# Optimization experiments

Hardware: AMD Instinct MI355X
Metric: run time of the kernel (lower is better)

The kernel has to match this reference:

```python
import jax, jax.numpy as jnp
import numpy as np

EPS = 1e-4


def setup_inputs() -> dict:
    key = jax.random.key(0)
    k1, k2, k3, k4, k5 = jax.random.split(key, 5)
    N, M, F = 2048, 2048, 128
    embeds = jax.random.uniform(k1, (N, F), dtype=jnp.float32)
    base_embeds = jax.random.normal(k2, (M, F), dtype=jnp.float32)
    base_rewards = jax.random.normal(k3, (M,), dtype=jnp.float32)
    # torch Linear(num_feat, num_feat, bias=False) / Linear(num_feat, 1, bias=False)
    # stored here as [in, out] for x @ W convention
    W1 = jax.random.normal(k4, (F, F), dtype=jnp.float32) / np.sqrt(F)
    w2 = jax.random.normal(k5, (F, 1), dtype=jnp.float32) / np.sqrt(F)
    return {"embeds": embeds, "base_embeds": base_embeds,
            "base_rewards": base_rewards, "W1": W1, "w2": w2}


def reference(embeds, base_embeds, base_rewards, W1, w2):
    # pairwise differences: [N, M, F]
    diff = embeds[:, None, :] - base_embeds[None, :, :]
    # tiny MLP distance kernel: Linear -> ELU -> Linear, abs
    h = jax.nn.elu(jnp.einsum('nmf,fg->nmg', diff, W1))
    dist = jnp.abs(jnp.einsum('nmg,go->nmo', h, w2)[:, :, 0])  # [N, M]
    # inverse-distance normalized weights
    dist_w = 1.0 / (dist + EPS)
    dist_w = dist_w / jnp.sum(dist_w, axis=1, keepdims=True)
    rewards = jnp.sum(dist_w * base_rewards[None, :], axis=1)  # [N]
    return rewards
```

## Files before the change

kernel.cpp:

```cpp
#include <hip/hip_runtime.h>
#include <hip/hip_bf16.h>

#define F      128
#define NROWS  2048
#define MROWS  2048
#define MT     32
#define LOG2E  1.44269504088896340736f

typedef float f32x4 __attribute__((ext_vector_type(4)));

__global__ __launch_bounds__(256) void proj_kernel(
    const float* __restrict__ embeds, const float* __restrict__ base,
    const float* __restrict__ W1, const float* __restrict__ w2,
    float* __restrict__ PA, float* __restrict__ BT4,
    float* __restrict__ w2sum)
{
    const int tid = threadIdx.x;
    const int sub = tid >> 7;
    const int g   = tid & 127;
    const int row = blockIdx.x * 2 + sub;

    __shared__ float xs[2][F];
    {
        const float* src = (row < NROWS) ? &embeds[(size_t)row * F]
                                         : &base[(size_t)(row - NROWS) * F];
        xs[sub][g] = src[g];
    }
    __syncthreads();

    float acc = 0.0f;
#pragma unroll 8
    for (int f = 0; f < F; ++f)
        acc = fmaf(xs[sub][f], W1[f * F + g], acc);

    const float wv = w2[g];
    const int   ch = g >> 3, o = g & 7;
    if (row < NROWS) {
        float* dst = PA + (size_t)row * 256 + ch * 16 + o;
        dst[0] = (acc + 1.0f) * wv;
        dst[8] = __builtin_amdgcn_exp2f(acc * LOG2E) * wv;
    } else {
        const int m  = row - NROWS;
        const int f0 = o, f1 = 8 + o;
        BT4[((size_t)(ch * 4 + (f0 >> 2)) * 2048 + m) * 4 + (f0 & 3)] = -acc * wv;
        BT4[((size_t)(ch * 4 + (f1 >> 2)) * 2048 + m) * 4 + (f1 & 3)] =
            __builtin_amdgcn_exp2f(-acc * LOG2E);
    }

    if (blockIdx.x == 0 && tid < 64) {
        float s = w2[tid] + w2[tid + 64];
#pragma unroll
        for (int k = 1; k < 64; k <<= 1) s += __shfl_xor(s, k);
        if (tid == 0) *w2sum = s;
    }
}

__global__ __launch_bounds__(256, 4) void pair_kernel(
    const float* __restrict__ PA, const float* __restrict__ BT4,
    const float* __restrict__ w2, const float* __restrict__ w2sum_p,
    const float* __restrict__ brew, float* __restrict__ partials)
{
    const int lane = threadIdx.x & 63;
    const int wv   = __builtin_amdgcn_readfirstlane(threadIdx.x >> 6);
    const int nt   = blockIdx.x, mt = blockIdx.y;
    const int n0   = nt * 32 + wv * 8;
    const int m0   = mt * 64;

    const float* bbase = BT4 + (size_t)(m0 + lane) * 4;

    float acc[8];
#pragma unroll
    for (int r = 0; r < 8; ++r) acc[r] = 0.0f;

    f32x4 rB[4], rBn[4];
#pragma unroll
    for (int q = 0; q < 4; ++q)
        rB[q] = *(const f32x4*)&bbase[(size_t)q * 8192];

#pragma unroll 1
    for (int ch = 0; ch < 16; ++ch) {
        if (ch < 15) {
#pragma unroll
            for (int q = 0; q < 4; ++q)
                rBn[q] = *(const f32x4*)&bbase[(size_t)((ch + 1) * 4 + q) * 8192];
        }
        const float* w2c = w2 + ch * 8;
        const float w0 = w2c[0], w1 = w2c[1], w2_ = w2c[2], w3 = w2c[3];
        const float w4 = w2c[4], w5 = w2c[5], w6 = w2c[6], w7 = w2c[7];

#pragma unroll
        for (int r = 0; r < 8; ++r) {
            const float* ar = PA + (size_t)(n0 + r) * 256 + ch * 16;
            const f32x4 a10 = *(const f32x4*)&ar[0];
            const f32x4 a11 = *(const f32x4*)&ar[4];
            const f32x4 ae0 = *(const f32x4*)&ar[8];
            const f32x4 ae1 = *(const f32x4*)&ar[12];

            const float s0 = __builtin_amdgcn_fmed3f(a10[0] + rB[0][0], ae0[0] * rB[2][0], w0);
            const float s1 = __builtin_amdgcn_fmed3f(a10[1] + rB[0][1], ae0[1] * rB[2][1], w1);
            const float s2 = __builtin_amdgcn_fmed3f(a10[2] + rB[0][2], ae0[2] * rB[2][2], w2_);
            const float s3 = __builtin_amdgcn_fmed3f(a10[3] + rB[0][3], ae0[3] * rB[2][3], w3);
            const float s4 = __builtin_amdgcn_fmed3f(a11[0] + rB[1][0], ae1[0] * rB[3][0], w4);
            const float s5 = __builtin_amdgcn_fmed3f(a11[1] + rB[1][1], ae1[1] * rB[3][1], w5);
            const float s6 = __builtin_amdgcn_fmed3f(a11[2] + rB[1][2], ae1[2] * rB[3][2], w6);
            const float s7 = __builtin_amdgcn_fmed3f(a11[3] + rB[1][3], ae1[3] * rB[3][3], w7);
            acc[r] += ((s0 + s1) + (s2 + s3)) + ((s4 + s5) + (s6 + s7));
        }
#pragma unroll
        for (int q = 0; q < 4; ++q) rB[q] = rBn[q];
    }

    const float w2sum = *w2sum_p;
    const float rv    = brew[m0 + lane];

#pragma unroll
    for (int r = 0; r < 8; ++r) {
        const float dist = fabsf(acc[r] - w2sum);
        const float wgt  = 1.0f / (dist + 1e-4f);
        float sw  = wgt;
        float swr = wgt * rv;
#pragma unroll
        for (int k = 1; k < 64; k <<= 1) {
            sw  += __shfl_xor(sw, k);
            swr += __shfl_xor(swr, k);
        }
        if (lane == 0) {
            const int n = n0 + r;
            partials[((size_t)n * MT + mt) * 2 + 0] = sw;
            partials[((size_t)n * MT + mt) * 2 + 1] = swr;
        }
    }
}

__global__ __launch_bounds__(256) void finalize_kernel(
    const float* __restrict__ partials, float* __restrict__ out)
{
    const int n = blockIdx.x * 256 + threadIdx.x;
    if (n < NROWS) {
        float sw = 0.0f, swr = 0.0f;
#pragma unroll
        for (int t = 0; t < MT; ++t) {
            sw  += partials[((size_t)n * MT + t) * 2 + 0];
            swr += partials[((size_t)n * MT + t) * 2 + 1];
        }
        out[n] = swr / sw;
    }
}

extern "C" void kernel_launch(void* const* d_in, const int* in_sizes, int n_in,
                              void* d_out, int out_size, void* d_ws, size_t ws_size,
                              hipStream_t stream)
{
    const float* embeds       = (const float*)d_in[0];
    const float* base_embeds  = (const float*)d_in[1];
    const float* base_rewards = (const float*)d_in[2];
    const float* W1           = (const float*)d_in[3];
    const float* w2           = (const float*)d_in[4];
    float* out = (float*)d_out;

    float* partials = (float*)d_ws;
    float* PA  = partials + (size_t)NROWS * MT * 2;
    float* BT4 = PA + (size_t)NROWS * 256;
    float* w2s = BT4 + (size_t)64 * 2048 * 4;

    proj_kernel<<<(NROWS + MROWS) / 2, 256, 0, stream>>>(
        embeds, base_embeds, W1, w2, PA, BT4, w2s);

    dim3 grid2(NROWS / 32, MROWS / 64);
    pair_kernel<<<grid2, 256, 0, stream>>>(PA, BT4, w2, w2s, base_rewards, partials);

    finalize_kernel<<<(NROWS + 255) / 256, 256, 0, stream>>>(partials, out);
}
```

Measured before the change: 83.59 us.

## Retile pair kernel to 4x4 register micro-tiles with LDS-staged A via global_load_lds

Restructures the pairwise kernel so each lane computes a 4x4 block of (n,m) pairs instead of 8 rows by one column. A-side rows are staged into per-wave double-buffered LDS with direct global-to-LDS loads, and B is loaded in split halves and software-pipelined across chunks. Each block now covers 64x64 pairs, and the reduction uses 16-lane shuffles. The aim is to cut redundant global loads of PA and raise arithmetic intensity, at the cost of more registers, explicit vmcnt waits and a more complex LDS indexing scheme.

```diff
diff --git a/kernel.cpp b/kernel.cpp
--- a/kernel.cpp
+++ b/kernel.cpp
@@ -8,6 +8,12 @@
 #define LOG2E  1.44269504088896340736f
 
 typedef float f32x4 __attribute__((ext_vector_type(4)));
+
+__device__ __forceinline__ void gload16(const float* g, float* l) {
+    __builtin_amdgcn_global_load_lds(
+        (const __attribute__((address_space(1))) void*)g,
+        (__attribute__((address_space(3))) void*)l, 16, 0, 0);
+}
 
 __global__ __launch_bounds__(256) void proj_kernel(
     const float* __restrict__ embeds, const float* __restrict__ base,
@@ -60,72 +66,112 @@
     const float* __restrict__ w2, const float* __restrict__ w2sum_p,
     const float* __restrict__ brew, float* __restrict__ partials)
 {
-    const int lane = threadIdx.x & 63;
-    const int wv   = __builtin_amdgcn_readfirstlane(threadIdx.x >> 6);
-    const int nt   = blockIdx.x, mt = blockIdx.y;
-    const int n0   = nt * 32 + wv * 8;
-    const int m0   = mt * 64;
-
-    const float* bbase = BT4 + (size_t)(m0 + lane) * 4;
-
-    float acc[8];
-#pragma unroll
-    for (int r = 0; r < 8; ++r) acc[r] = 0.0f;
-
-    f32x4 rB[4], rBn[4];
-#pragma unroll
-    for (int q = 0; q < 4; ++q)
-        rB[q] = *(const f32x4*)&bbase[(size_t)q * 8192];
+    __shared__ float slds[4 * 640];
+
+    const int tid = threadIdx.x;
+    const int w   = tid >> 6, l = tid & 63;
+    const int nt  = blockIdx.x, mt = blockIdx.y;
+    const int n0  = nt * 64,    m0 = mt * 64;
+    const int trl = (l >> 4) & 3;
+    const int tc  = l & 15;
+    const int wbase = w * 640;
+
+    const float* sA0;
+    const float* sA1;
+    {
+        const int s = l, r = s / 5;
+        int rs = s - r * 5; if (rs == 4) rs = 0;
+        sA0 = PA + (size_t)(n0 + 4 * w + (r & 3) + 16 * (r >> 2)) * 256 + rs * 4;
+    }
+    {
+        const int s = 64 + l, r = s / 5;
+        int rs = s - r * 5; if (rs == 4) rs = 0;
+        sA1 = PA + (size_t)(n0 + 4 * w + (r & 3) + 16 * (r >> 2)) * 256 + rs * 4;
+    }
+
+#define STAGE_A(CH, BUF) {                                                     \
+    float* db = &slds[wbase + (BUF) * 320];                                    \
+    gload16(sA0 + (CH) * 16, db);                                              \
+    if (l < 16) gload16(sA1 + (CH) * 16, db + 256); }
+
+    const float* bcol = BT4 + (size_t)(m0 + tc) * 4;
+#define LOADB(D1, DE, CH, H) {                                                 \
+    _Pragma("unroll")                                                          \
+    for (int j = 0; j < 4; ++j) {                                              \
+        D1[j] = *(const f32x4*)&bcol[(size_t)((CH) * 4 + (H)) * 8192 + 64 * j];     \
+        DE[j] = *(const f32x4*)&bcol[(size_t)((CH) * 4 + 2 + (H)) * 8192 + 64 * j]; \
+    } }
+
+    float acc[4][4];
+#pragma unroll
+    for (int i = 0; i < 4; ++i)
+#pragma unroll
+        for (int j = 0; j < 4; ++j) acc[i][j] = 0.0f;
+
+#define COMPUTE_H(CH, H, B1, BE, BUF) {                                        \
+    const float wq0 = w2[(CH) * 8 + (H) * 4 + 0];                              \
+    const float wq1 = w2[(CH) * 8 + (H) * 4 + 1];                              \
+    const float wq2 = w2[(CH) * 8 + (H) * 4 + 2];                              \
+    const float wq3 = w2[(CH) * 8 + (H) * 4 + 3];                              \
+    _Pragma("unroll")                                                          \
+    for (int i = 0; i < 4; ++i) {                                              \
+        const float* ap = &slds[wbase + (BUF) * 320 + (i * 4 + trl) * 20 + (H) * 4]; \
+        const f32x4 a1 = *(const f32x4*)ap;                                    \
+        const f32x4 ae = *(const f32x4*)(ap + 8);                              \
+        _Pragma("unroll")                                                      \
+        for (int j = 0; j < 4; ++j) {                                          \
+            const float s0 = __builtin_amdgcn_fmed3f(a1[0] + B1[j][0], ae[0] * BE[j][0], wq0); \
+            const float s1 = __builtin_amdgcn_fmed3f(a1[1] + B1[j][1], ae[1] * BE[j][1], wq1); \
+            const float s2 = __builtin_amdgcn_fmed3f(a1[2] + B1[j][2], ae[2] * BE[j][2], wq2); \
+            const float s3 = __builtin_amdgcn_fmed3f(a1[3] + B1[j][3], ae[3] * BE[j][3], wq3); \
+            acc[i][j] += (s0 + s1) + (s2 + s3);                                \
+        }                                                                      \
+    } }
+
+    f32x4 bX1[4], bXe[4], bY1[4], bYe[4];
+
+    LOADB(bX1, bXe, 0, 0)
+    STAGE_A(0, 0)
+    asm volatile("s_waitcnt vmcnt(0)" ::: "memory");
 
 #pragma unroll 1
     for (int ch = 0; ch < 16; ++ch) {
-        if (ch < 15) {
-#pragma unroll
-            for (int q = 0; q < 4; ++q)
-                rBn[q] = *(const f32x4*)&bbase[(size_t)((ch + 1) * 4 + q) * 8192];
-        }
-        const float* w2c = w2 + ch * 8;
-        const float w0 = w2c[0], w1 = w2c[1], w2_ = w2c[2], w3 = w2c[3];
-        const float w4 = w2c[4], w5 = w2c[5], w6 = w2c[6], w7 = w2c[7];
-
-#pragma unroll
-        for (int r = 0; r < 8; ++r) {
-            const float* ar = PA + (size_t)(n0 + r) * 256 + ch * 16;
-            const f32x4 a10 = *(const f32x4*)&ar[0];
-            const f32x4 a11 = *(const f32x4*)&ar[4];
-            const f32x4 ae0 = *(const f32x4*)&ar[8];
-            const f32x4 ae1 = *(const f32x4*)&ar[12];
-
-            const float s0 = __builtin_amdgcn_fmed3f(a10[0] + rB[0][0], ae0[0] * rB[2][0], w0);
-            const float s1 = __builtin_amdgcn_fmed3f(a10[1] + rB[0][1], ae0[1] * rB[2][1], w1);
-            const float s2 = __builtin_amdgcn_fmed3f(a10[2] + rB[0][2], ae0[2] * rB[2][2], w2_);
-            const float s3 = __builtin_amdgcn_fmed3f(a10[3] + rB[0][3], ae0[3] * rB[2][3], w3);
-            const float s4 = __builtin_amdgcn_fmed3f(a11[0] + rB[1][0], ae1[0] * rB[3][0], w4);
-            const float s5 = __builtin_amdgcn_fmed3f(a11[1] + rB[1][1], ae1[1] * rB[3][1], w5);
-            const float s6 = __builtin_amdgcn_fmed3f(a11[2] + rB[1][2], ae1[2] * rB[3][2], w6);
-            const float s7 = __builtin_amdgcn_fmed3f(a11[3] + rB[1][3], ae1[3] * rB[3][3], w7);
-            acc[r] += ((s0 + s1) + (s2 + s3)) + ((s4 + s5) + (s6 + s7));
-        }
-#pragma unroll
-        for (int q = 0; q < 4; ++q) rB[q] = rBn[q];
-    }
+        const int buf = ch & 1;
+        const int chn = (ch + 1 < 16) ? ch + 1 : 15;
+        STAGE_A(chn, buf ^ 1)
+        LOADB(bY1, bYe, ch, 1)
+        COMPUTE_H(ch, 0, bX1, bXe, buf)
+        LOADB(bX1, bXe, chn, 0)
+        COMPUTE_H(ch, 1, bY1, bYe, buf)
+        asm volatile("" :: "v"(bX1[0]), "v"(bX1[1]), "v"(bX1[2]), "v"(bX1[3]));
+        asm volatile("s_waitcnt vmcnt(0)" ::: "memory");
+    }
+#undef COMPUTE_H
+#undef LOADB
+#undef STAGE_A
 
     const float w2sum = *w2sum_p;
-    const float rv    = brew[m0 + lane];
-
-#pragma unroll
-    for (int r = 0; r < 8; ++r) {
-        const float dist = fabsf(acc[r] - w2sum);
-        const float wgt  = 1.0f / (dist + 1e-4f);
-        float sw  = wgt;
-        float swr = wgt * rv;
-#pragma unroll
-        for (int k = 1; k < 64; k <<= 1) {
+    float rsv[4];
+#pragma unroll
+    for (int j = 0; j < 4; ++j) rsv[j] = brew[m0 + tc + 16 * j];
+
+#pragma unroll
+    for (int i = 0; i < 4; ++i) {
+        float sw = 0.0f, swr = 0.0f;
+#pragma unroll
+        for (int j = 0; j < 4; ++j) {
+            const float dist = fabsf(acc[i][j] - w2sum);
+            const float wgt  = 1.0f / (dist + 1e-4f);
+            sw += wgt;
+            swr = fmaf(wgt, rsv[j], swr);
+        }
+#pragma unroll
+        for (int k = 1; k < 16; k <<= 1) {
             sw  += __shfl_xor(sw, k);
             swr += __shfl_xor(swr, k);
         }
-        if (lane == 0) {
-            const int n = n0 + r;
+        if (tc == 0) {
+            const int n = n0 + 4 * w + trl + 16 * i;
             partials[((size_t)n * MT + mt) * 2 + 0] = sw;
             partials[((size_t)n * MT + mt) * 2 + 1] = swr;
         }
@@ -166,7 +212,7 @@
     proj_kernel<<<(NROWS + MROWS) / 2, 256, 0, stream>>>(
         embeds, base_embeds, W1, w2, PA, BT4, w2s);
 
-    dim3 grid2(NROWS / 32, MROWS / 64);
+    dim3 grid2(NROWS / 64, MROWS / 64);
     pair_kernel<<<grid2, 256, 0, stream>>>(PA, BT4, w2, w2s, base_rewards, partials);
 
     finalize_kernel<<<(NROWS + 255) / 256, 256, 0, stream>>>(partials, out);
```

Result: slower. 217.7 us (+160.4%).
